# Kernel optimization log

Measured on AMD Instinct MI355X. Metric: run time of the kernel, lower is better.

## Reference

```python
import jax, jax.numpy as jnp
import numpy as np

DIM = 256
N_NODES = 2000
BATCH = 64


def _build_tree(n, seed=0):
    # Contiguous-children encoding: struct[i] = (ch_start, ch_end) or (-1,-1) for leaves.
    # Children indices are always > parent index (BFS frontier allocation).
    rng = np.random.default_rng(seed)
    struct = np.full((n, 2), -1, dtype=np.int32)
    ptr = 1
    i = 0
    while ptr < n:
        k = int(rng.integers(0, 5))
        if i + 1 >= ptr:  # keep the frontier non-empty
            k = max(k, 1)
        k = min(k, n - ptr)
        if k > 0:
            struct[i] = (ptr, ptr + k)
            ptr += k
        i += 1
    return struct


def _level_schedule(struct):
    # depth 0 = leaves; parent depth = 1 + max(child depths). Children idx > parent idx.
    n = struct.shape[0]
    depth = np.zeros(n, dtype=np.int64)
    for i in range(n - 1, -1, -1):
        s, e = struct[i]
        if s != -1:
            depth[i] = 1 + depth[s:e].max()
    return [np.nonzero(depth == d)[0] for d in range(int(depth.max()) + 1)]


def setup_inputs() -> dict:
    key = jax.random.key(0)
    ks = jax.random.split(key, 3)
    struct = _build_tree(N_NODES)
    structure = jnp.asarray(np.broadcast_to(struct, (BATCH, N_NODES, 2)).copy())
    features = jax.random.normal(ks[0], (BATCH, N_NODES, DIM), dtype=jnp.float32)
    s_in = (2.0 / (DIM + DIM)) ** 0.5        # glorot-ish scale
    s_inner = (2.0 / (3 * DIM + DIM)) ** 0.5
    W_in = jax.random.normal(ks[1], (DIM, DIM), dtype=jnp.float32) * s_in
    b_in = jnp.zeros((DIM,), jnp.float32)
    W_inner = jax.random.normal(ks[2], (3 * DIM, DIM), dtype=jnp.float32) * s_inner
    b_inner = jnp.zeros((DIM,), jnp.float32)
    return {"structure": structure, "features": features, "W_in": W_in,
            "b_in": b_in, "W_inner": W_inner, "b_inner": b_inner}


def reference(structure, features, W_in, b_in, W_inner, b_inner):
    # Tree structure (int) is a compile-time constant: derive a level schedule host-side,
    # then run one batched segment-reduction + Dense per tree level (deepest first).
    struct = np.asarray(structure[0])  # shared across batch
    levels = _level_schedule(struct)
    B, N, dim = features.shape
    state = jnp.zeros((B, N, dim), features.dtype)

    # Leaves: sigmoid Dense on own features (all features are finite/valid here).
    leaves = levels[0]
    state = state.at[:, leaves].set(jax.nn.sigmoid(features[:, leaves] @ W_in + b_in))

    for nodes in levels[1:]:
        starts, ends = struct[nodes, 0], struct[nodes, 1]
        counts = ends - starts
        child_ids = np.concatenate([np.arange(s, e) for s, e in zip(starts, ends)])
        seg = np.repeat(np.arange(len(nodes)), counts)
        L = len(nodes)
        cs = state[:, child_ids].transpose(1, 0, 2)          # [C, B, dim]
        ssum = jax.ops.segment_sum(cs, seg, num_segments=L)  # [L, B, dim]
        smin = jax.ops.segment_min(cs, seg, num_segments=L)
        feat = features[:, nodes].transpose(1, 0, 2)         # node's own feature joins pooling
        cnt = jnp.asarray(counts + 1, features.dtype)[:, None, None]
        c_mean = (ssum + feat) / cnt
        c_min = jnp.minimum(smin, feat)
        # NOTE: the source computes c_max with reduce_mean (bug) -> kept for fidelity.
        h = jnp.concatenate([c_mean, c_mean, c_min], axis=-1)  # [L, B, 3*dim]
        new = jax.nn.sigmoid(h @ W_inner + b_inner)
        state = state.at[:, nodes].set(new.transpose(1, 0, 2))

    return state[:, 0]  # just_root_output=True -> [B, dim]
```

## Files before the change

kernel.cpp:

```cpp
#include <hip/hip_runtime.h>

#define NNODES 2000
#define BATCH  64
#define DIM    256
#define GRID   256
#define BLOCK  256

typedef __attribute__((ext_vector_type(8))) short  v8s;
typedef __attribute__((ext_vector_type(8))) __bf16 v8bf;
typedef __attribute__((ext_vector_type(4))) float  v4f;
typedef __attribute__((ext_vector_type(4))) int    v4i;

__device__ __forceinline__ short f2bf(float f) {
  unsigned u = __builtin_bit_cast(unsigned, f);
  u += 0x7FFFu + ((u >> 16) & 1u);
  return (short)(u >> 16);
}
__device__ __forceinline__ float bf2f(short s) {
  unsigned u = ((unsigned)(unsigned short)s) << 16;
  return __builtin_bit_cast(float, u);
}
__device__ __forceinline__ v4f mfma16(v8s a, v8s b, v4f c) {
  return __builtin_amdgcn_mfma_f32_16x16x32_bf16(
      __builtin_bit_cast(v8bf, a), __builtin_bit_cast(v8bf, b), c, 0, 0, 0);
}
__device__ __forceinline__ float sigmoidf(float x) {
  return __builtin_amdgcn_rcpf(1.0f + __builtin_amdgcn_exp2f(-1.4426950408889634f * x));
}

__global__ void prep_kernel(const float* __restrict__ W_in, const float* __restrict__ W_inner,
                            short* __restrict__ Wt_in, short* __restrict__ Wt_inner,
                            int* __restrict__ done) {
  int idx = blockIdx.x * blockDim.x + threadIdx.x;
  int stride = gridDim.x * blockDim.x;
  for (int i = idx; i < 256 * 256; i += stride) {
    int j = i >> 8, k = i & 255;
    Wt_in[j * 256 + k] = f2bf(W_in[k * 256 + j]);
  }
  for (int i = idx; i < 256 * 512; i += stride) {
    int j = i >> 9, k = i & 511;
    float v = W_inner[(k + 256) * 256 + j];
    if (k < 256) v += W_inner[k * 256 + j];
    Wt_inner[j * 512 + k] = f2bf(v);
  }
  for (int i = idx; i < 2 * NNODES; i += stride)
    __hip_atomic_store(&done[i], 0, __ATOMIC_RELAXED, __HIP_MEMORY_SCOPE_AGENT);
}

__launch_bounds__(BLOCK, 1)
__global__ void tree_kernel(const int* __restrict__ structure, const float* __restrict__ features,
                            const float* __restrict__ b_in, const float* __restrict__ b_inner,
                            const short* __restrict__ Wt_in, const short* __restrict__ Wt_inner,
                            short* __restrict__ state, int* done, float* __restrict__ out) {
  __shared__ short Xs[32 * 512];

  const int tid  = threadIdx.x;
  const int wave = tid >> 6;
  const int lane = tid & 63;
  const int ln15 = lane & 15;
  const int quad = lane >> 4;
  const int rl3  = ln15 & 7;

  const int bl  = tid >> 3;
  const int d0  = (tid & 7) << 5;
  const int swb = bl & 7;

  float bia_in[4], bia_nn[4];
  #pragma unroll
  for (int nt = 0; nt < 4; ++nt) {
    const int j = wave * 64 + nt * 16 + ln15;
    bia_in[nt] = b_in[j];
    bia_nn[nt] = b_inner[j];
  }

  for (int node = NNODES - 1 - (int)blockIdx.x; node >= 0; node -= GRID) {
    const int s = structure[2 * node];
    const int e = structure[2 * node + 1];
    const bool leaf = (s < 0);
    const int nc = e - s;
    const int K = leaf ? 256 : 512;
    const short* __restrict__ W = leaf ? Wt_in : Wt_inner;

    for (int half = 0; half < 2; ++half) {
      if (!leaf && wave == 0 && lane < nc) {
        int g = 0;
        while (__hip_atomic_load(&done[2 * (s + lane) + half],
                                 __ATOMIC_RELAXED, __HIP_MEMORY_SCOPE_AGENT) == 0 &&
               g < (1 << 22)) {
          __builtin_amdgcn_s_sleep(1); ++g;
        }
      }
      __syncthreads();

      const int b = half * 32 + bl;
      const float* __restrict__ fp = features + ((size_t)b * NNODES + node) * DIM + d0;
      if (leaf) {
        #pragma unroll
        for (int d = 0; d < 32; d += 8) {
          const float4 f0 = *(const float4*)(fp + d);
          const float4 f1 = *(const float4*)(fp + d + 4);
          v8s o;
          o[0] = f2bf(f0.x); o[1] = f2bf(f0.y); o[2] = f2bf(f0.z); o[3] = f2bf(f0.w);
          o[4] = f2bf(f1.x); o[5] = f2bf(f1.y); o[6] = f2bf(f1.z); o[7] = f2bf(f1.w);
          const int ch = (d0 + d) >> 3;
          *(v8s*)&Xs[(bl << 9) + ((ch ^ swb) << 3)] = o;
        }
      } else {
        v4i cb[4][4];
        #pragma unroll
        for (int ci = 0; ci < 4; ++ci) {
          if (ci < nc) {
            const short* cp = state + ((size_t)(s + ci) * BATCH + b) * DIM + d0;
            #pragma unroll
            for (int dq = 0; dq < 4; ++dq)
              asm volatile("global_load_dwordx4 %0, %1, off sc0 sc1"
                           : "=v"(cb[ci][dq]) : "v"(cp + dq * 8));
          }
        }
        asm volatile("s_waitcnt vmcnt(0)" ::: "memory");
        __builtin_amdgcn_sched_barrier(0);

        const float inv = 1.0f / (float)(nc + 1);
        #pragma unroll
        for (int dq = 0; dq < 4; ++dq) {
          const float4 f0 = *(const float4*)(fp + dq * 8);
          const float4 f1 = *(const float4*)(fp + dq * 8 + 4);
          float sm[8] = {f0.x, f0.y, f0.z, f0.w, f1.x, f1.y, f1.z, f1.w};
          float mn[8];
          #pragma unroll
          for (int q = 0; q < 8; ++q) mn[q] = sm[q];
          #pragma unroll
          for (int ci = 0; ci < 4; ++ci) {
            if (ci < nc) {
              const v8s cv = __builtin_bit_cast(v8s, cb[ci][dq]);
              #pragma unroll
              for (int q = 0; q < 8; ++q) {
                const float v = bf2f(cv[q]);
                sm[q] += v; mn[q] = fminf(mn[q], v);
              }
            }
          }
          v8s om, on;
          #pragma unroll
          for (int q = 0; q < 8; ++q) { om[q] = f2bf(sm[q] * inv); on[q] = f2bf(mn[q]); }
          const int ch = (d0 + dq * 8) >> 3;
          *(v8s*)&Xs[(bl << 9) + ((ch ^ swb) << 3)]        = om;
          *(v8s*)&Xs[(bl << 9) + (((ch + 32) ^ swb) << 3)] = on;
        }
      }
      __syncthreads();

      v4f acc[2][4];
      #pragma unroll
      for (int mt = 0; mt < 2; ++mt)
        #pragma unroll
        for (int nt = 0; nt < 4; ++nt) acc[mt][nt] = v4f{0.f, 0.f, 0.f, 0.f};

      const short* __restrict__ Wp = W + (wave * 64 + ln15) * K + quad * 8;
      const int nkc = K >> 5;
      v8s bcur[4];
      #pragma unroll
      for (int nt = 0; nt < 4; ++nt) bcur[nt] = *(const v8s*)(Wp + nt * 16 * K);
      for (int kc = 0; kc < nkc; ++kc) {
        const int kn = (kc + 1 < nkc) ? kc + 1 : kc;
        v8s bnxt[4];
        #pragma unroll
        for (int nt = 0; nt < 4; ++nt) bnxt[nt] = *(const v8s*)(Wp + nt * 16 * K + kn * 32);
        v8s af[2];
        #pragma unroll
        for (int mt = 0; mt < 2; ++mt) {
          const int r = mt * 16 + ln15;
          af[mt] = *(const v8s*)&Xs[(r << 9) + (((kc * 4 + quad) ^ rl3) << 3)];
        }
        #pragma unroll
        for (int mt = 0; mt < 2; ++mt)
          #pragma unroll
          for (int nt = 0; nt < 4; ++nt)
            acc[mt][nt] = mfma16(af[mt], bcur[nt], acc[mt][nt]);
        #pragma unroll
        for (int nt = 0; nt < 4; ++nt) bcur[nt] = bnxt[nt];
      }

      #pragma unroll
      for (int mt = 0; mt < 2; ++mt) {
        #pragma unroll
        for (int nt = 0; nt < 4; ++nt) {
          const int j = wave * 64 + nt * 16 + ln15;
          const float bs = leaf ? bia_in[nt] : bia_nn[nt];
          #pragma unroll
          for (int r = 0; r < 4; ++r) {
            const int bb = half * 32 + mt * 16 + quad * 4 + r;
            const float v = sigmoidf(acc[mt][nt][r] + bs);
            short* sp = state + ((size_t)node * BATCH + bb) * DIM + j;
            const int hv = (int)(unsigned short)f2bf(v);
            asm volatile("global_store_short %0, %1, off sc0 sc1" :: "v"(sp), "v"(hv));
            if (node == 0) out[bb * DIM + j] = v;
          }
        }
      }

      asm volatile("s_waitcnt vmcnt(0)" ::: "memory");
      __syncthreads();
      if (tid == 0)
        __hip_atomic_store(&done[2 * node + half], 1,
                           __ATOMIC_RELAXED, __HIP_MEMORY_SCOPE_AGENT);
    }
  }
}

extern "C" void kernel_launch(void* const* d_in, const int* in_sizes, int n_in,
                              void* d_out, int out_size, void* d_ws, size_t ws_size,
                              hipStream_t stream) {
  const int*   structure = (const int*)d_in[0];
  const float* features  = (const float*)d_in[1];
  const float* W_in      = (const float*)d_in[2];
  const float* b_in      = (const float*)d_in[3];
  const float* W_inner   = (const float*)d_in[4];
  const float* b_inner   = (const float*)d_in[5];
  float* out = (float*)d_out;

  char* ws = (char*)d_ws;
  short* state = (short*)ws;
  size_t off = (size_t)NNODES * BATCH * DIM * 2;
  short* Wt_in = (short*)(ws + off);    off += 256 * 256 * 2;
  short* Wt_inner = (short*)(ws + off); off += 512 * 256 * 2;
  int* done = (int*)(ws + off);

  prep_kernel<<<dim3(256), dim3(256), 0, stream>>>(W_in, W_inner, Wt_in, Wt_inner, done);

  void* args[9];
  args[0] = (void*)&structure;
  args[1] = (void*)&features;
  args[2] = (void*)&b_in;
  args[3] = (void*)&b_inner;
  args[4] = (void*)&Wt_in;
  args[5] = (void*)&Wt_inner;
  args[6] = (void*)&state;
  args[7] = (void*)&done;
  args[8] = (void*)&out;
  hipLaunchCooperativeKernel((void*)tree_kernel, dim3(GRID), dim3(BLOCK), args, 0, stream);
}
```

Measured before the change: 454.0 us.

## Split each node into independent half-batch work items over more, smaller blocks

Each node's two batch halves become separate work items handed out over a grid sized from occupancy (up to 1024 blocks of 128 threads, two per CU). Each wave now computes 128 output columns instead of 64. The first feature row is prefetched before the dependency spin-wait. The aim is more parallelism across the tree and hiding of dependency latency, at the cost of more register pressure per wave and more items waiting on children.

```diff
diff --git a/kernel.cpp b/kernel.cpp
--- a/kernel.cpp
+++ b/kernel.cpp
@@ -3,8 +3,8 @@
 #define NNODES 2000
 #define BATCH  64
 #define DIM    256
-#define GRID   256
-#define BLOCK  256
+#define BLOCK  128
+#define MAXGRID 1024
 
 typedef __attribute__((ext_vector_type(8))) short  v8s;
 typedef __attribute__((ext_vector_type(8))) __bf16 v8bf;
@@ -47,7 +47,7 @@
     __hip_atomic_store(&done[i], 0, __ATOMIC_RELAXED, __HIP_MEMORY_SCOPE_AGENT);
 }
 
-__launch_bounds__(BLOCK, 1)
+__launch_bounds__(BLOCK, 2)
 __global__ void tree_kernel(const int* __restrict__ structure, const float* __restrict__ features,
                             const float* __restrict__ b_in, const float* __restrict__ b_inner,
                             const short* __restrict__ Wt_in, const short* __restrict__ Wt_inner,
@@ -65,15 +65,17 @@
   const int d0  = (tid & 7) << 5;
   const int swb = bl & 7;
 
-  float bia_in[4], bia_nn[4];
+  float bia_in[8], bia_nn[8];
   #pragma unroll
-  for (int nt = 0; nt < 4; ++nt) {
-    const int j = wave * 64 + nt * 16 + ln15;
+  for (int nt = 0; nt < 8; ++nt) {
+    const int j = wave * 128 + nt * 16 + ln15;
     bia_in[nt] = b_in[j];
     bia_nn[nt] = b_inner[j];
   }
 
-  for (int node = NNODES - 1 - (int)blockIdx.x; node >= 0; node -= GRID) {
+  for (int item = 2 * NNODES - 1 - (int)blockIdx.x; item >= 0; item -= (int)gridDim.x) {
+    const int node = item >> 1;
+    const int half = item & 1;
     const int s = structure[2 * node];
     const int e = structure[2 * node + 1];
     const bool leaf = (s < 0);
@@ -81,29 +83,36 @@
     const int K = leaf ? 256 : 512;
     const short* __restrict__ W = leaf ? Wt_in : Wt_inner;
 
-    for (int half = 0; half < 2; ++half) {
-      if (!leaf && wave == 0 && lane < nc) {
-        int g = 0;
-        while (__hip_atomic_load(&done[2 * (s + lane) + half],
-                                 __ATOMIC_RELAXED, __HIP_MEMORY_SCOPE_AGENT) == 0 &&
-               g < (1 << 22)) {
-          __builtin_amdgcn_s_sleep(1); ++g;
-        }
-      }
-      __syncthreads();
-
-      const int b = half * 32 + bl;
+    const float* __restrict__ fp0 = features + ((size_t)(half * 32 + bl) * NNODES + node) * DIM + d0;
+    float4 pre[8];
+    #pragma unroll
+    for (int q = 0; q < 8; ++q) pre[q] = ((const float4*)fp0)[q];
+
+    if (!leaf && wave == 0 && lane < nc) {
+      int g = 0;
+      while (__hip_atomic_load(&done[2 * (s + lane) + half],
+                               __ATOMIC_RELAXED, __HIP_MEMORY_SCOPE_AGENT) == 0 &&
+             g < (1 << 22)) {
+        __builtin_amdgcn_s_sleep(1); ++g;
+      }
+    }
+    __syncthreads();
+
+    #pragma unroll
+    for (int rr = 0; rr < 2; ++rr) {
+      const int row = rr * 16 + bl;
+      const int b   = half * 32 + row;
       const float* __restrict__ fp = features + ((size_t)b * NNODES + node) * DIM + d0;
       if (leaf) {
         #pragma unroll
-        for (int d = 0; d < 32; d += 8) {
-          const float4 f0 = *(const float4*)(fp + d);
-          const float4 f1 = *(const float4*)(fp + d + 4);
+        for (int dq = 0; dq < 4; ++dq) {
+          const float4 f0 = rr ? ((const float4*)fp)[2 * dq]     : pre[2 * dq];
+          const float4 f1 = rr ? ((const float4*)fp)[2 * dq + 1] : pre[2 * dq + 1];
           v8s o;
           o[0] = f2bf(f0.x); o[1] = f2bf(f0.y); o[2] = f2bf(f0.z); o[3] = f2bf(f0.w);
           o[4] = f2bf(f1.x); o[5] = f2bf(f1.y); o[6] = f2bf(f1.z); o[7] = f2bf(f1.w);
-          const int ch = (d0 + d) >> 3;
-          *(v8s*)&Xs[(bl << 9) + ((ch ^ swb) << 3)] = o;
+          const int ch = (d0 + dq * 8) >> 3;
+          *(v8s*)&Xs[(row << 9) + ((ch ^ swb) << 3)] = o;
         }
       } else {
         v4i cb[4][4];
@@ -123,8 +132,8 @@
         const float inv = 1.0f / (float)(nc + 1);
         #pragma unroll
         for (int dq = 0; dq < 4; ++dq) {
-          const float4 f0 = *(const float4*)(fp + dq * 8);
-          const float4 f1 = *(const float4*)(fp + dq * 8 + 4);
+          const float4 f0 = rr ? ((const float4*)fp)[2 * dq]     : pre[2 * dq];
+          const float4 f1 = rr ? ((const float4*)fp)[2 * dq + 1] : pre[2 * dq + 1];
           float sm[8] = {f0.x, f0.y, f0.z, f0.w, f1.x, f1.y, f1.z, f1.w};
           float mn[8];
           #pragma unroll
@@ -144,67 +153,67 @@
           #pragma unroll
           for (int q = 0; q < 8; ++q) { om[q] = f2bf(sm[q] * inv); on[q] = f2bf(mn[q]); }
           const int ch = (d0 + dq * 8) >> 3;
-          *(v8s*)&Xs[(bl << 9) + ((ch ^ swb) << 3)]        = om;
-          *(v8s*)&Xs[(bl << 9) + (((ch + 32) ^ swb) << 3)] = on;
-        }
-      }
-      __syncthreads();
-
-      v4f acc[2][4];
+          *(v8s*)&Xs[(row << 9) + ((ch ^ swb) << 3)]        = om;
+          *(v8s*)&Xs[(row << 9) + (((ch + 32) ^ swb) << 3)] = on;
+        }
+      }
+    }
+    __syncthreads();
+
+    v4f acc[2][8];
+    #pragma unroll
+    for (int mt = 0; mt < 2; ++mt)
+      #pragma unroll
+      for (int nt = 0; nt < 8; ++nt) acc[mt][nt] = v4f{0.f, 0.f, 0.f, 0.f};
+
+    const short* __restrict__ Wp = W + (size_t)(wave * 128 + ln15) * K + quad * 8;
+    const int nkc = K >> 5;
+    v8s bcur[8];
+    #pragma unroll
+    for (int nt = 0; nt < 8; ++nt) bcur[nt] = *(const v8s*)(Wp + (size_t)nt * 16 * K);
+    for (int kc = 0; kc < nkc; ++kc) {
+      const int kn = (kc + 1 < nkc) ? kc + 1 : kc;
+      v8s bnxt[8];
+      #pragma unroll
+      for (int nt = 0; nt < 8; ++nt) bnxt[nt] = *(const v8s*)(Wp + (size_t)nt * 16 * K + kn * 32);
+      v8s af[2];
+      #pragma unroll
+      for (int mt = 0; mt < 2; ++mt) {
+        const int r = mt * 16 + ln15;
+        af[mt] = *(const v8s*)&Xs[(r << 9) + (((kc * 4 + quad) ^ rl3) << 3)];
+      }
       #pragma unroll
       for (int mt = 0; mt < 2; ++mt)
         #pragma unroll
-        for (int nt = 0; nt < 4; ++nt) acc[mt][nt] = v4f{0.f, 0.f, 0.f, 0.f};
-
-      const short* __restrict__ Wp = W + (wave * 64 + ln15) * K + quad * 8;
-      const int nkc = K >> 5;
-      v8s bcur[4];
-      #pragma unroll
-      for (int nt = 0; nt < 4; ++nt) bcur[nt] = *(const v8s*)(Wp + nt * 16 * K);
-      for (int kc = 0; kc < nkc; ++kc) {
-        const int kn = (kc + 1 < nkc) ? kc + 1 : kc;
-        v8s bnxt[4];
-        #pragma unroll
-        for (int nt = 0; nt < 4; ++nt) bnxt[nt] = *(const v8s*)(Wp + nt * 16 * K + kn * 32);
-        v8s af[2];
-        #pragma unroll
-        for (int mt = 0; mt < 2; ++mt) {
-          const int r = mt * 16 + ln15;
-          af[mt] = *(const v8s*)&Xs[(r << 9) + (((kc * 4 + quad) ^ rl3) << 3)];
-        }
-        #pragma unroll
-        for (int mt = 0; mt < 2; ++mt)
-          #pragma unroll
-          for (int nt = 0; nt < 4; ++nt)
-            acc[mt][nt] = mfma16(af[mt], bcur[nt], acc[mt][nt]);
-        #pragma unroll
-        for (int nt = 0; nt < 4; ++nt) bcur[nt] = bnxt[nt];
-      }
-
-      #pragma unroll
-      for (int mt = 0; mt < 2; ++mt) {
-        #pragma unroll
-        for (int nt = 0; nt < 4; ++nt) {
-          const int j = wave * 64 + nt * 16 + ln15;
-          const float bs = leaf ? bia_in[nt] : bia_nn[nt];
-          #pragma unroll
-          for (int r = 0; r < 4; ++r) {
-            const int bb = half * 32 + mt * 16 + quad * 4 + r;
-            const float v = sigmoidf(acc[mt][nt][r] + bs);
-            short* sp = state + ((size_t)node * BATCH + bb) * DIM + j;
-            const int hv = (int)(unsigned short)f2bf(v);
-            asm volatile("global_store_short %0, %1, off sc0 sc1" :: "v"(sp), "v"(hv));
-            if (node == 0) out[bb * DIM + j] = v;
-          }
-        }
-      }
-
-      asm volatile("s_waitcnt vmcnt(0)" ::: "memory");
-      __syncthreads();
-      if (tid == 0)
-        __hip_atomic_store(&done[2 * node + half], 1,
-                           __ATOMIC_RELAXED, __HIP_MEMORY_SCOPE_AGENT);
-    }
+        for (int nt = 0; nt < 8; ++nt)
+          acc[mt][nt] = mfma16(af[mt], bcur[nt], acc[mt][nt]);
+      #pragma unroll
+      for (int nt = 0; nt < 8; ++nt) bcur[nt] = bnxt[nt];
+    }
+
+    #pragma unroll
+    for (int mt = 0; mt < 2; ++mt) {
+      #pragma unroll
+      for (int nt = 0; nt < 8; ++nt) {
+        const int j = wave * 128 + nt * 16 + ln15;
+        const float bs = leaf ? bia_in[nt] : bia_nn[nt];
+        #pragma unroll
+        for (int r = 0; r < 4; ++r) {
+          const int bb = half * 32 + mt * 16 + quad * 4 + r;
+          const float v = sigmoidf(acc[mt][nt][r] + bs);
+          short* sp = state + ((size_t)node * BATCH + bb) * DIM + j;
+          const int hv = (int)(unsigned short)f2bf(v);
+          asm volatile("global_store_short %0, %1, off sc0 sc1" :: "v"(sp), "v"(hv));
+          if (node == 0) out[bb * DIM + j] = v;
+        }
+      }
+    }
+
+    asm volatile("s_waitcnt vmcnt(0)" ::: "memory");
+    __syncthreads();
+    if (tid == 0)
+      __hip_atomic_store(&done[2 * node + half], 1,
+                         __ATOMIC_RELAXED, __HIP_MEMORY_SCOPE_AGENT);
   }
 }
 
@@ -228,6 +237,17 @@
 
   prep_kernel<<<dim3(256), dim3(256), 0, stream>>>(W_in, W_inner, Wt_in, Wt_inner, done);
 
+  static int coop_grid = 0;
+  if (coop_grid == 0) {
+    int nb = 0;
+    hipError_t err = hipOccupancyMaxActiveBlocksPerMultiprocessor(
+        &nb, reinterpret_cast<const void*>(tree_kernel), BLOCK, 0);
+    if (err != hipSuccess || nb < 1) nb = 1;
+    long g = (long)nb * 256;
+    if (g > MAXGRID) g = MAXGRID;
+    coop_grid = (int)g;
+  }
+
   void* args[9];
   args[0] = (void*)&structure;
   args[1] = (void*)&features;
@@ -238,5 +258,5 @@
   args[6] = (void*)&state;
   args[7] = (void*)&done;
   args[8] = (void*)&out;
-  hipLaunchCooperativeKernel((void*)tree_kernel, dim3(GRID), dim3(BLOCK), args, 0, stream);
-}
+  hipLaunchCooperativeKernel((void*)tree_kernel, dim3(coop_grid), dim3(BLOCK), args, 0, stream);
+}
```

Measured after the change: 452.1 us. No clear change (-0.4%).
